# Optimization experiments

Hardware: AMD Instinct MI355X
Metric: run time of the kernel (lower is better)

Reference implementation:

```python
import jax, jax.numpy as jnp
import numpy as np


def setup_inputs() -> dict:
    key = jax.random.key(0)
    k1, k2, k3, k4 = jax.random.split(key, 4)
    B, Q, D, H = 8, 512, 4096, 1024
    return {
        "query_embeddings": jax.random.normal(k1, (B, Q, H), dtype=jnp.float32),
        "document_embeddings": jax.random.normal(k2, (B, D, H), dtype=jnp.float32),
        "attention_mask": jax.random.randint(k3, (B, D), 0, 2, dtype=jnp.int32),
        "proj_w": jax.random.normal(k4, (H, H), dtype=jnp.float32) * (H ** -0.5),
        "proj_b": jnp.zeros((H,), dtype=jnp.float32),
    }


def reference(query_embeddings, document_embeddings, attention_mask, proj_w, proj_b):
    H = query_embeddings.shape[-1]
    scale = 1.0 / jnp.sqrt(jnp.asarray(H, dtype=query_embeddings.dtype))
    # Linear projection of queries: [B, Q, H]
    q = jnp.einsum("bqh,hk->bqk", query_embeddings, proj_w) + proj_b
    # Scores: [B, Q, D]
    scores = jnp.einsum("bqh,bdh->bqd", q, document_embeddings) * scale
    # Mask: [B, 1, D]; masked positions -> -inf before softmax
    mask = attention_mask[:, None, :] != 0
    scores = jnp.where(mask, scores, -jnp.inf)
    attention_weights = jax.nn.softmax(scores, axis=-1)
    # Weighted sum over docs: [B, Q, H]
    retrieved_docs = jnp.einsum("bqd,bdh->bqh", attention_weights, document_embeddings)
    return (retrieved_docs, attention_weights)
```

## Files before the change

### kernel.cpp

```cpp
#include <hip/hip_runtime.h>

#define BATCH 8
#define QLEN 512
#define DLEN 4096
#define HDIM 1024

typedef __attribute__((ext_vector_type(8))) short bf16x8;
typedef __attribute__((ext_vector_type(4))) float f32x4;
typedef __attribute__((ext_vector_type(4))) short s16x4;

__device__ __forceinline__ short f2bf(float f) {
    union { float f; unsigned u; } x; x.f = f;
    unsigned r = x.u + 0x7fffu + ((x.u >> 16) & 1u);
    return (short)(r >> 16);
}

__device__ __forceinline__ void gload_lds16(const void* g, void* l) {
    __builtin_amdgcn_global_load_lds(
        (const __attribute__((address_space(1))) unsigned int*)g,
        (__attribute__((address_space(3))) unsigned int*)l,
        16, 0, 0);
}

__global__ void cvt_f32_bf16(const float* __restrict__ in, short* __restrict__ out, int n4) {
    int i = blockIdx.x * blockDim.x + threadIdx.x;
    int stride = gridDim.x * blockDim.x;
    for (; i < n4; i += stride) {
        float4 x = ((const float4*)in)[i];
        s16x4 o = { f2bf(x.x), f2bf(x.y), f2bf(x.z), f2bf(x.w) };
        ((s16x4*)out)[i] = o;
    }
}

__global__ void transpose_w(const float* __restrict__ W, short* __restrict__ Wt) {
    __shared__ float t[32][33];
    const int hb = blockIdx.y * 32, kb = blockIdx.x * 32;
    #pragma unroll
    for (int i = 0; i < 4; ++i) {
        int h = threadIdx.y + i * 8;
        t[h][threadIdx.x] = W[(size_t)(hb + h) * HDIM + kb + threadIdx.x];
    }
    __syncthreads();
    #pragma unroll
    for (int i = 0; i < 4; ++i) {
        int k = threadIdx.y + i * 8;
        Wt[(size_t)(kb + k) * HDIM + hb + threadIdx.x] = f2bf(t[threadIdx.x][k]);
    }
}

__global__ void prep_docs(const float* __restrict__ docs,
                          short* __restrict__ docsB, short* __restrict__ docsT) {
    __shared__ float t[32][33];
    const int b = blockIdx.z;
    const int h0 = blockIdx.x * 32, d0 = blockIdx.y * 32;
    const float* src = docs + ((size_t)b * DLEN + d0) * HDIM + h0;
    #pragma unroll
    for (int i = 0; i < 4; ++i) {
        int d = threadIdx.y + i * 8;
        float v = src[(size_t)d * HDIM + threadIdx.x];
        t[d][threadIdx.x] = v;
        docsB[((size_t)b * DLEN + d0 + d) * HDIM + h0 + threadIdx.x] = f2bf(v);
    }
    __syncthreads();
    #pragma unroll
    for (int i = 0; i < 4; ++i) {
        int h = threadIdx.y + i * 8;
        docsT[((size_t)b * HDIM + h0 + h) * DLEN + d0 + threadIdx.x] = f2bf(t[threadIdx.x][h]);
    }
}

#define BM 128
#define BN 128
#define BK 32

template<int EPI>
__global__ void gemm_bt(const short* __restrict__ A, const short* __restrict__ B,
                        void* __restrict__ Cv, const float* __restrict__ bias,
                        float scale, int M, int N, int K,
                        long long aB, long long bB, long long cB) {
    __shared__ short As[BM * BK];
    __shared__ short Bs[BN * BK];
    const int tid  = threadIdx.x;
    const int lane = tid & 63;
    const int wv   = tid >> 6;
    const int wr   = wv >> 1, wc = wv & 1;
    const size_t rowBase = (size_t)blockIdx.y * BM;
    const size_t colBase = (size_t)blockIdx.x * BN;
    const short* Ab = A + (size_t)blockIdx.z * aB;
    const short* Bb = B + (size_t)blockIdx.z * bB;

    f32x4 acc[4][4];
    #pragma unroll
    for (int m = 0; m < 4; ++m)
        #pragma unroll
        for (int n = 0; n < 4; ++n)
            acc[m][n] = (f32x4){0.f, 0.f, 0.f, 0.f};

    const int c0 = tid, c1 = 256 + tid;
    const int r0 = c0 >> 2, k0 = (c0 & 3) << 3;
    const int r1 = c1 >> 2, k1 = (c1 & 3) << 3;
    const int lr = lane & 15;
    const int lk = (lane >> 4) << 3;

    for (int kt = 0; kt < K; kt += BK) {
        gload_lds16(Ab + (rowBase + r0) * K + kt + k0, As + c0 * 8);
        gload_lds16(Ab + (rowBase + r1) * K + kt + k1, As + c1 * 8);
        gload_lds16(Bb + (colBase + r0) * K + kt + k0, Bs + c0 * 8);
        gload_lds16(Bb + (colBase + r1) * K + kt + k1, Bs + c1 * 8);
        __syncthreads();

        bf16x8 af[4], bfr[4];
        #pragma unroll
        for (int m = 0; m < 4; ++m)
            af[m] = *(const bf16x8*)(As + (wr * 64 + m * 16 + lr) * BK + lk);
        #pragma unroll
        for (int n = 0; n < 4; ++n)
            bfr[n] = *(const bf16x8*)(Bs + (wc * 64 + n * 16 + lr) * BK + lk);

        #pragma unroll
        for (int m = 0; m < 4; ++m)
            #pragma unroll
            for (int n = 0; n < 4; ++n)
                acc[m][n] = __builtin_amdgcn_mfma_f32_16x16x32_bf16(af[m], bfr[n], acc[m][n], 0, 0, 0);
        __syncthreads();
    }

    const int orow = (lane >> 4) << 2;
    const int ocol = lane & 15;
    #pragma unroll
    for (int n = 0; n < 4; ++n) {
        const size_t col = colBase + wc * 64 + n * 16 + ocol;
        const float bv = (EPI == 0) ? bias[col] : 0.f;
        #pragma unroll
        for (int m = 0; m < 4; ++m) {
            const size_t rbase = rowBase + wr * 64 + m * 16 + orow;
            #pragma unroll
            for (int j = 0; j < 4; ++j) {
                const float v = acc[m][n][j];
                const size_t off = (size_t)blockIdx.z * cB + (rbase + j) * (size_t)N + col;
                if (EPI == 0)      ((short*)Cv)[off] = f2bf(v + bv);
                else if (EPI == 1) ((float*)Cv)[off] = v * scale;
                else               ((float*)Cv)[off] = v;
            }
        }
    }
}

__global__ void softmax_rows(const float* __restrict__ scores, const int* __restrict__ mask,
                             float* __restrict__ attnF, short* __restrict__ attnB) {
    const int row = blockIdx.x;
    const int b   = row >> 9;
    const int tid = threadIdx.x;
    const int lane = tid & 63;
    const int wv = tid >> 6;
    const float4* S  = (const float4*)(scores + (size_t)row * DLEN);
    const int4*   Mk = (const int4*)(mask + (size_t)b * DLEN);
    __shared__ float red[8];

    float v[16];
    float mx = -INFINITY;
    #pragma unroll
    for (int i = 0; i < 4; ++i) {
        float4 s = S[i * 256 + tid];
        int4   m = Mk[i * 256 + tid];
        v[i * 4 + 0] = m.x ? s.x : -INFINITY;
        v[i * 4 + 1] = m.y ? s.y : -INFINITY;
        v[i * 4 + 2] = m.z ? s.z : -INFINITY;
        v[i * 4 + 3] = m.w ? s.w : -INFINITY;
        #pragma unroll
        for (int c = 0; c < 4; ++c) mx = fmaxf(mx, v[i * 4 + c]);
    }
    #pragma unroll
    for (int o = 32; o > 0; o >>= 1) mx = fmaxf(mx, __shfl_xor(mx, o));
    if (lane == 0) red[wv] = mx;
    __syncthreads();
    mx = fmaxf(fmaxf(red[0], red[1]), fmaxf(red[2], red[3]));

    float sum = 0.f;
    #pragma unroll
    for (int i = 0; i < 16; ++i) {
        float e = __expf(v[i] - mx);
        v[i] = e;
        sum += e;
    }
    #pragma unroll
    for (int o = 32; o > 0; o >>= 1) sum += __shfl_xor(sum, o);
    __syncthreads();
    if (lane == 0) red[4 + wv] = sum;
    __syncthreads();
    sum = red[4] + red[5] + red[6] + red[7];
    const float inv = 1.0f / sum;

    float4* OF = (float4*)(attnF + (size_t)row * DLEN);
    s16x4*  OB = (s16x4*)(attnB + (size_t)row * DLEN);
    #pragma unroll
    for (int i = 0; i < 4; ++i) {
        float4 w;
        w.x = v[i * 4 + 0] * inv;
        w.y = v[i * 4 + 1] * inv;
        w.z = v[i * 4 + 2] * inv;
        w.w = v[i * 4 + 3] * inv;
        OF[i * 256 + tid] = w;
        s16x4 o = { f2bf(w.x), f2bf(w.y), f2bf(w.z), f2bf(w.w) };
        OB[i * 256 + tid] = o;
    }
}

extern "C" void kernel_launch(void* const* d_in, const int* in_sizes, int n_in,
                              void* d_out, int out_size, void* d_ws, size_t ws_size,
                              hipStream_t stream) {
    const float* qe   = (const float*)d_in[0];
    const float* docs = (const float*)d_in[1];
    const int*   mask = (const int*)d_in[2];
    const float* pw   = (const float*)d_in[3];
    const float* pb   = (const float*)d_in[4];

    float* outRet  = (float*)d_out;
    float* outAttn = outRet + (size_t)BATCH * QLEN * HDIM;

    char* ws = (char*)d_ws;
    short* qeB   = (short*)(ws + 0);
    short* wt    = (short*)(ws + 8388608);
    short* qpB   = (short*)(ws + 10485760);
    short* docsB = (short*)(ws + 18874368);
    short* docsT = (short*)(ws + 85983232);
    float* scor  = (float*)(ws + 153092096);
    short* attnB = (short*)(ws + 220200960);

    cvt_f32_bf16<<<dim3(1024), dim3(256), 0, stream>>>(qe, qeB, (BATCH * QLEN * HDIM) / 4);
    transpose_w<<<dim3(32, 32), dim3(32, 8), 0, stream>>>(pw, wt);
    prep_docs<<<dim3(32, 128, 8), dim3(32, 8), 0, stream>>>(docs, docsB, docsT);

    gemm_bt<0><<<dim3(HDIM / BN, (BATCH * QLEN) / BM, 1), dim3(256), 0, stream>>>(
        qeB, wt, (void*)qpB, pb, 1.f, BATCH * QLEN, HDIM, HDIM, 0LL, 0LL, 0LL);

    gemm_bt<1><<<dim3(DLEN / BN, QLEN / BM, BATCH), dim3(256), 0, stream>>>(
        qpB, docsB, (void*)scor, nullptr, 0.03125f, QLEN, DLEN, HDIM,
        (long long)QLEN * HDIM, (long long)DLEN * HDIM, (long long)QLEN * DLEN);

    softmax_rows<<<dim3(BATCH * QLEN), dim3(256), 0, stream>>>(scor, mask, outAttn, attnB);

    gemm_bt<2><<<dim3(HDIM / BN, QLEN / BM, BATCH), dim3(256), 0, stream>>>(
        attnB, docsT, (void*)outRet, nullptr, 1.f, QLEN, HDIM, DLEN,
        (long long)QLEN * DLEN, (long long)HDIM * DLEN, (long long)QLEN * HDIM);
}
```

Baseline: 470.2 us.

## Split-K the final GEMM, widen BK with swizzled LDS, vectorize doc prep

```diff
diff --git a/kernel.cpp b/kernel.cpp
--- a/kernel.cpp
+++ b/kernel.cpp
@@ -50,33 +50,41 @@
 
 __global__ void prep_docs(const float* __restrict__ docs,
                           short* __restrict__ docsB, short* __restrict__ docsT) {
-    __shared__ float t[32][33];
+    __shared__ float t[64][65];
     const int b = blockIdx.z;
-    const int h0 = blockIdx.x * 32, d0 = blockIdx.y * 32;
+    const int h0 = blockIdx.x * 64, d0 = blockIdx.y * 64;
+    const int tq = threadIdx.x & 15;
+    const int tr = threadIdx.x >> 4;
     const float* src = docs + ((size_t)b * DLEN + d0) * HDIM + h0;
     #pragma unroll
     for (int i = 0; i < 4; ++i) {
-        int d = threadIdx.y + i * 8;
-        float v = src[(size_t)d * HDIM + threadIdx.x];
-        t[d][threadIdx.x] = v;
-        docsB[((size_t)b * DLEN + d0 + d) * HDIM + h0 + threadIdx.x] = f2bf(v);
-    }
-    __syncthreads();
-    #pragma unroll
-    for (int i = 0; i < 4; ++i) {
-        int h = threadIdx.y + i * 8;
-        docsT[((size_t)b * HDIM + h0 + h) * DLEN + d0 + threadIdx.x] = f2bf(t[threadIdx.x][h]);
+        int d = tr + i * 16;
+        float4 v = *(const float4*)(src + (size_t)d * HDIM + tq * 4);
+        t[d][tq * 4 + 0] = v.x;
+        t[d][tq * 4 + 1] = v.y;
+        t[d][tq * 4 + 2] = v.z;
+        t[d][tq * 4 + 3] = v.w;
+        s16x4 o = { f2bf(v.x), f2bf(v.y), f2bf(v.z), f2bf(v.w) };
+        *(s16x4*)(docsB + ((size_t)b * DLEN + d0 + d) * HDIM + h0 + tq * 4) = o;
+    }
+    __syncthreads();
+    #pragma unroll
+    for (int i = 0; i < 4; ++i) {
+        int h = tr + i * 16;
+        s16x4 o = { f2bf(t[tq * 4 + 0][h]), f2bf(t[tq * 4 + 1][h]),
+                    f2bf(t[tq * 4 + 2][h]), f2bf(t[tq * 4 + 3][h]) };
+        *(s16x4*)(docsT + ((size_t)b * HDIM + h0 + h) * DLEN + d0 + tq * 4) = o;
     }
 }
 
 #define BM 128
 #define BN 128
-#define BK 32
+#define BK 64
 
 template<int EPI>
 __global__ void gemm_bt(const short* __restrict__ A, const short* __restrict__ B,
                         void* __restrict__ Cv, const float* __restrict__ bias,
-                        float scale, int M, int N, int K,
+                        float scale, int N, int Kstride, int Kloop, int kOffStep,
                         long long aB, long long bB, long long cB) {
     __shared__ short As[BM * BK];
     __shared__ short Bs[BN * BK];
@@ -86,8 +94,11 @@
     const int wr   = wv >> 1, wc = wv & 1;
     const size_t rowBase = (size_t)blockIdx.y * BM;
     const size_t colBase = (size_t)blockIdx.x * BN;
-    const short* Ab = A + (size_t)blockIdx.z * aB;
-    const short* Bb = B + (size_t)blockIdx.z * bB;
+    const int z = blockIdx.z;
+    const int bb = z & 7;
+    const int kOff = (z >> 3) * kOffStep;
+    const short* Ag = A + (size_t)bb * aB + kOff;
+    const short* Bg = B + (size_t)bb * bB + kOff;
 
     f32x4 acc[4][4];
     #pragma unroll
@@ -96,32 +107,47 @@
         for (int n = 0; n < 4; ++n)
             acc[m][n] = (f32x4){0.f, 0.f, 0.f, 0.f};
 
-    const int c0 = tid, c1 = 256 + tid;
-    const int r0 = c0 >> 2, k0 = (c0 & 3) << 3;
-    const int r1 = c1 >> 2, k1 = (c1 & 3) << 3;
+    const short* aSrc[4]; const short* bSrc[4]; short* aDst[4]; short* bDst[4];
+    #pragma unroll
+    for (int i = 0; i < 4; ++i) {
+        const int c = tid + 256 * i;
+        const int r = c >> 3, cc = c & 7;
+        const int gk = (cc ^ (r & 7)) << 3;
+        aSrc[i] = Ag + (rowBase + r) * (size_t)Kstride + gk;
+        bSrc[i] = Bg + (colBase + r) * (size_t)Kstride + gk;
+        aDst[i] = As + c * 8;
+        bDst[i] = Bs + c * 8;
+    }
     const int lr = lane & 15;
     const int lk = (lane >> 4) << 3;
 
-    for (int kt = 0; kt < K; kt += BK) {
-        gload_lds16(Ab + (rowBase + r0) * K + kt + k0, As + c0 * 8);
-        gload_lds16(Ab + (rowBase + r1) * K + kt + k1, As + c1 * 8);
-        gload_lds16(Bb + (colBase + r0) * K + kt + k0, Bs + c0 * 8);
-        gload_lds16(Bb + (colBase + r1) * K + kt + k1, Bs + c1 * 8);
+    for (int kt = 0; kt < Kloop; kt += BK) {
+        #pragma unroll
+        for (int i = 0; i < 4; ++i) gload_lds16(aSrc[i] + kt, aDst[i]);
+        #pragma unroll
+        for (int i = 0; i < 4; ++i) gload_lds16(bSrc[i] + kt, bDst[i]);
         __syncthreads();
 
-        bf16x8 af[4], bfr[4];
-        #pragma unroll
-        for (int m = 0; m < 4; ++m)
-            af[m] = *(const bf16x8*)(As + (wr * 64 + m * 16 + lr) * BK + lk);
-        #pragma unroll
-        for (int n = 0; n < 4; ++n)
-            bfr[n] = *(const bf16x8*)(Bs + (wc * 64 + n * 16 + lr) * BK + lk);
-
-        #pragma unroll
-        for (int m = 0; m < 4; ++m)
-            #pragma unroll
-            for (int n = 0; n < 4; ++n)
-                acc[m][n] = __builtin_amdgcn_mfma_f32_16x16x32_bf16(af[m], bfr[n], acc[m][n], 0, 0, 0);
+        #pragma unroll
+        for (int kk = 0; kk < 2; ++kk) {
+            const int chunkL = (kk * 32 + lk) >> 3;
+            bf16x8 af[4], bfr[4];
+            #pragma unroll
+            for (int m = 0; m < 4; ++m) {
+                const int row = wr * 64 + m * 16 + lr;
+                af[m] = *(const bf16x8*)(As + row * BK + ((chunkL ^ (row & 7)) << 3));
+            }
+            #pragma unroll
+            for (int n = 0; n < 4; ++n) {
+                const int row = wc * 64 + n * 16 + lr;
+                bfr[n] = *(const bf16x8*)(Bs + row * BK + ((chunkL ^ (row & 7)) << 3));
+            }
+            #pragma unroll
+            for (int m = 0; m < 4; ++m)
+                #pragma unroll
+                for (int n = 0; n < 4; ++n)
+                    acc[m][n] = __builtin_amdgcn_mfma_f32_16x16x32_bf16(af[m], bfr[n], acc[m][n], 0, 0, 0);
+        }
         __syncthreads();
     }
 
@@ -137,12 +163,31 @@
             #pragma unroll
             for (int j = 0; j < 4; ++j) {
                 const float v = acc[m][n][j];
-                const size_t off = (size_t)blockIdx.z * cB + (rbase + j) * (size_t)N + col;
+                const size_t off = (size_t)z * cB + (rbase + j) * (size_t)N + col;
                 if (EPI == 0)      ((short*)Cv)[off] = f2bf(v + bv);
                 else if (EPI == 1) ((float*)Cv)[off] = v * scale;
                 else               ((float*)Cv)[off] = v;
             }
         }
+    }
+}
+
+__global__ void reduce4(const float* __restrict__ p, float* __restrict__ out, int n4) {
+    int i = blockIdx.x * blockDim.x + threadIdx.x;
+    const int stride = gridDim.x * blockDim.x;
+    const float4* p4 = (const float4*)p;
+    float4* o4 = (float4*)out;
+    for (; i < n4; i += stride) {
+        float4 a = p4[i];
+        float4 b = p4[i + 1048576];
+        float4 c = p4[i + 2097152];
+        float4 d = p4[i + 3145728];
+        float4 r;
+        r.x = a.x + b.x + c.x + d.x;
+        r.y = a.y + b.y + c.y + d.y;
+        r.z = a.z + b.z + c.z + d.z;
+        r.w = a.w + b.w + c.w + d.w;
+        o4[i] = r;
     }
 }
 
@@ -229,18 +274,21 @@
 
     cvt_f32_bf16<<<dim3(1024), dim3(256), 0, stream>>>(qe, qeB, (BATCH * QLEN * HDIM) / 4);
     transpose_w<<<dim3(32, 32), dim3(32, 8), 0, stream>>>(pw, wt);
-    prep_docs<<<dim3(32, 128, 8), dim3(32, 8), 0, stream>>>(docs, docsB, docsT);
+    prep_docs<<<dim3(HDIM / 64, DLEN / 64, BATCH), dim3(256), 0, stream>>>(docs, docsB, docsT);
 
     gemm_bt<0><<<dim3(HDIM / BN, (BATCH * QLEN) / BM, 1), dim3(256), 0, stream>>>(
-        qeB, wt, (void*)qpB, pb, 1.f, BATCH * QLEN, HDIM, HDIM, 0LL, 0LL, 0LL);
+        qeB, wt, (void*)qpB, pb, 1.f, HDIM, HDIM, HDIM, 0,
+        0LL, 0LL, 0LL);
 
     gemm_bt<1><<<dim3(DLEN / BN, QLEN / BM, BATCH), dim3(256), 0, stream>>>(
-        qpB, docsB, (void*)scor, nullptr, 0.03125f, QLEN, DLEN, HDIM,
+        qpB, docsB, (void*)scor, nullptr, 0.03125f, DLEN, HDIM, HDIM, 0,
         (long long)QLEN * HDIM, (long long)DLEN * HDIM, (long long)QLEN * DLEN);
 
     softmax_rows<<<dim3(BATCH * QLEN), dim3(256), 0, stream>>>(scor, mask, outAttn, attnB);
 
-    gemm_bt<2><<<dim3(HDIM / BN, QLEN / BM, BATCH), dim3(256), 0, stream>>>(
-        attnB, docsT, (void*)outRet, nullptr, 1.f, QLEN, HDIM, DLEN,
+    gemm_bt<2><<<dim3(HDIM / BN, QLEN / BM, BATCH * 4), dim3(256), 0, stream>>>(
+        attnB, docsT, (void*)scor, nullptr, 1.f, HDIM, DLEN, DLEN / 4, DLEN / 4,
         (long long)QLEN * DLEN, (long long)HDIM * DLEN, (long long)QLEN * HDIM);
-}
+
+    reduce4<<<dim3(2048), dim3(256), 0, stream>>>(scor, outRet, (BATCH * QLEN * HDIM) / 4);
+}
```

Result: faster. 434.2 us (-7.7%).
